# Performance work log

Measured on AMD Instinct MI355X. Metric: run time of the kernel, lower is better.

The kernel has to match this reference:

```python
import jax, jax.numpy as jnp
import numpy as np

# Config (from init_kwargs 'knn')
QUEUE_SIZE = 65536   # K
FEAT_DIM = 256       # D
BATCH = 512          # N (eval_sampling = 1.0 -> all samples used)
NUM_KNNS = 200
NUM_CLASSES = 1000
TEMPERATURE = 0.07


def _l2norm(x):
    return x / jnp.sqrt(jnp.sum(x * x, axis=-1, keepdims=True) + 1e-12)


def setup_inputs() -> dict:
    key = jax.random.key(0)
    k1, k2, k3, k4 = jax.random.split(key, 4)
    features = _l2norm(jax.random.normal(k1, (BATCH, FEAT_DIM), jnp.float32))
    labels = jax.random.randint(k2, (BATCH,), 0, NUM_CLASSES, jnp.int32)
    queue_features = _l2norm(jax.random.normal(k3, (QUEUE_SIZE, FEAT_DIM), jnp.float32))
    queue_labels = jax.random.randint(k4, (QUEUE_SIZE,), 0, NUM_CLASSES, jnp.int32)
    return {
        "features": features,
        "labels": labels,
        "queue_features": queue_features,
        "queue_labels": queue_labels,
        "queue_ptr": 0,
    }


def reference(features, labels, queue_features, queue_labels, queue_ptr):
    # ---- kNN accuracy (train branch, eval_sampling=1.0) ----
    sim = jnp.einsum('nc,kc->nk', features, queue_features)           # [N, K]
    sim_w, sim_idx = jax.lax.top_k(sim, k=NUM_KNNS)                   # [N, Kn]
    sim_w = jnp.exp(sim_w / TEMPERATURE)
    sim_labels = queue_labels[sim_idx]                                # [N, Kn] (vmapped gather)
    # weighted one-hot vote, expressed as a scatter-add (same math,
    # avoids the [N, Kn, C] one-hot intermediate)
    n = features.shape[0]
    pred_scores = jnp.zeros((n, NUM_CLASSES), sim_w.dtype)
    pred_scores = pred_scores.at[jnp.arange(n)[:, None], sim_labels].add(sim_w)
    pred_labels = jnp.argmax(pred_scores, axis=-1)
    accuracy = jnp.mean((pred_labels == labels).astype(jnp.float32))

    # ---- queue update (single device: all_gather == identity) ----
    batch_size = features.shape[0]
    inds = (jnp.arange(batch_size) + queue_ptr) % QUEUE_SIZE  # original asserts divisibility
    new_queue_features = queue_features.at[inds].set(features)
    new_queue_labels = queue_labels.at[inds].set(labels)
    new_queue_ptr = (queue_ptr + batch_size) % QUEUE_SIZE

    return accuracy, new_queue_features, new_queue_labels, new_queue_ptr
```

## Files before the change

### kernel.cpp

```cpp
#include <hip/hip_runtime.h>
#include <math.h>

#define NQ     65536
#define DIM    256
#define NBATCH 512
#define KNN    200
#define NCLS   1000
#define TSELF  0.155f
#define TSELH  0.150f
#define EPSF   0.0041f
#define BGUARD 22

#define GM  128
#define GK  32
#define NTN (NQ / GM)
#define KSTEPS (DIM / GK)

typedef unsigned short u16;
typedef unsigned long long u64;
typedef __attribute__((ext_vector_type(8))) short short8;
typedef __attribute__((ext_vector_type(4))) float f32x4;


__device__ __forceinline__ u16 f2bf(float x) {
  unsigned u = __float_as_uint(x);
  return (u16)((u + 0x7FFFu + ((u >> 16) & 1u)) >> 16);
}
__device__ __forceinline__ void load_lds16(const void* g, void* l) {
  __builtin_amdgcn_global_load_lds(
      (const __attribute__((address_space(1))) unsigned int*)g,
      (__attribute__((address_space(3))) unsigned int*)l, 16, 0, 0);
}
__device__ __forceinline__ void store_f4u(float* p, float4 v) {
  p[0] = v.x;
  *(float2*)(p + 1) = make_float2(v.y, v.z);
  p[3] = v.w;
}

__global__ __launch_bounds__(256) void prep_copy_kernel(
    const float* __restrict__ feat, const int* __restrict__ labels,
    const float* __restrict__ qf, const int* __restrict__ ql,
    const int* __restrict__ qptr,
    u16* __restrict__ Bb, u16* __restrict__ Ab,
    int* __restrict__ flag, float* __restrict__ out)
{
  const int idx = blockIdx.x * 256 + threadIdx.x;
  const int ptr = qptr[0];
  const long long NFEAT = (long long)NQ * DIM;

  {
    float4 qv = ((const float4*)qf)[idx];
    int row = idx >> 6;
    int c4  = idx & 63;
    int d = (row - ptr) & (NQ - 1);
    float4 ov = qv;
    if (d < NBATCH) ov = ((const float4*)feat)[d * 64 + c4];
    store_f4u(out + 1 + 4 * (long long)idx, ov);

    ushort4 h;
    h.x = f2bf(qv.x); h.y = f2bf(qv.y); h.z = f2bf(qv.z); h.w = f2bf(qv.w);
    ((ushort4*)Bb)[idx] = h;
  }

  if (idx < NBATCH * DIM / 4) {
    float4 v = ((const float4*)feat)[idx];
    ushort4 h;
    h.x = f2bf(v.x); h.y = f2bf(v.y); h.z = f2bf(v.z); h.w = f2bf(v.w);
    ((ushort4*)Ab)[idx] = h;
  }

  if (idx < NQ) {
    int d = (idx - ptr) & (NQ - 1);
    int v = (d < NBATCH) ? labels[d] : ql[idx];
    out[1 + NFEAT + idx] = (float)v;
  }

  if (idx < NBATCH) flag[idx] = 0;
  if (idx == 0) {
    out[0] = 0.0f;
    out[1 + NFEAT + NQ] = (float)((ptr + NBATCH) & (NQ - 1));
  }
}

__global__ __launch_bounds__(256) void gemm_mfma(
    const u16* __restrict__ A, const u16* __restrict__ B,
    uint2* __restrict__ cand, int* __restrict__ cnt2,
    int* __restrict__ flag, int SLOT)
{
  __shared__ u16 sA[2][GM][GK];
  __shared__ u16 sB[2][GM][GK];
  __shared__ int lcnt[GM];

  const int tid  = threadIdx.x;
  const int wave = tid >> 6, lane = tid & 63;
  const int d  = blockIdx.x;
  const int bm = (d >> 3) & 3;
  const int bn = (d & 7) | ((d >> 5) << 3);

  for (int i = tid; i < GM; i += 256) lcnt[i] = 0;

  const u16* srcBase = ((wave < 2) ? (A + (size_t)bm * GM * DIM)
                                   : (B + (size_t)bn * GM * DIM))
                       + (size_t)(wave & 1) * 64 * DIM;
  const int kx = ((lane & 3) ^ ((lane >> 3) & 3)) * 8;
  const u16* src = srcBase + (lane >> 2) * DIM + kx;
  u16* dst0 = ((wave < 2) ? &sA[0][0][0] : &sB[0][0][0]) + (wave & 1) * 64 * GK;
  u16* dst1 = ((wave < 2) ? &sA[1][0][0] : &sB[1][0][0]) + (wave & 1) * 64 * GK;

  const int wm = (wave & 1) * 64, wn = (wave >> 1) * 64;
  const int fr = lane & 15;
  const int fq = lane >> 4;
  const int fqx = fq ^ ((fr >> 1) & 3);

  f32x4 acc[4][4] = {};

  {
    const u16* s = src;
#pragma unroll
    for (int g = 0; g < 4; ++g)
      load_lds16(s + g * 16 * DIM, dst0 + g * 512);
  }
  __syncthreads();

  for (int t = 0; t < KSTEPS; ++t) {
    const int cur = t & 1;
    if (t + 1 < KSTEPS) {
      const u16* s = src + (t + 1) * GK;
      u16* dl = cur ? dst0 : dst1;
#pragma unroll
      for (int g = 0; g < 4; ++g)
        load_lds16(s + g * 16 * DIM, dl + g * 512);
    }

    short8 a[4], b[4];
#pragma unroll
    for (int i = 0; i < 4; ++i) {
      a[i] = *(const short8*)&sA[cur][wm + i * 16 + fr][fqx * 8];
      b[i] = *(const short8*)&sB[cur][wn + i * 16 + fr][fqx * 8];
    }
#pragma unroll
    for (int i = 0; i < 4; ++i)
#pragma unroll
      for (int j = 0; j < 4; ++j)
        acc[i][j] = __builtin_amdgcn_mfma_f32_16x16x32_bf16(a[i], b[j], acc[i][j], 0, 0, 0);

    __syncthreads();
  }

  const int lrow0 = wm + fq * 4;
  const int ccol  = bn * GM + wn + fr;
#pragma unroll
  for (int i = 0; i < 4; ++i)
#pragma unroll
    for (int j = 0; j < 4; ++j)
#pragma unroll
      for (int r = 0; r < 4; ++r) {
        float v = acc[i][j][r];
        if (v > TSELF) {
          int lr  = lrow0 + i * 16 + r;
          int col = ccol + j * 16;
          int p = atomicAdd(&lcnt[lr], 1);
          if (p < SLOT)
            cand[((size_t)(bm * GM + lr) * NTN + bn) * SLOT + p] =
                make_uint2(__float_as_uint(v), (unsigned)col);
          else
            flag[bm * GM + lr] = 1;
        }
      }
  __syncthreads();
  if (tid < GM) {
    int c = lcnt[tid];
    cnt2[(size_t)(bm * GM + tid) * NTN + bn] = c < SLOT ? c : SLOT;
  }
}

#define NBSEL 2048
#define CCAP  2048
#define MBCAP 256
#define LCAP  1024
#define NT    512
#define NG    (NT / 8)
#define BINW  ((1.001f - TSELH) / (float)NBSEL)

__global__ __launch_bounds__(NT, 4) void select_kernel(
    const uint2* __restrict__ cand, const int* __restrict__ cnt2,
    const int* __restrict__ flag, const int* __restrict__ labels,
    const int* __restrict__ qlab, const float* __restrict__ qf,
    const float* __restrict__ feat, float* __restrict__ out,
    float inv_n, int SLOT)
{
  __shared__ int   hist[NBSEL];
  __shared__ int   seg[NT];
  __shared__ float candV[CCAP];
  __shared__ int   candI[CCAP];
  __shared__ float votes[NCLS];
  __shared__ u64   bk[LCAP / 2];
  __shared__ float frow[DIM];
  __shared__ int   s_b, s_cnt, s_hi, s_mb;
  __shared__ u64   s_best;

  const int tid = threadIdx.x;
  const int row = blockIdx.x;

  bool fb = (flag[row] != 0);

  if (tid < DIM) frow[tid] = feat[(size_t)row * DIM + tid];
  for (int i = tid; i < NBSEL; i += NT) hist[i] = 0;
  for (int c = tid; c < NCLS; c += NT) votes[c] = 0.0f;
  if (tid == 0) { s_b = 0; s_cnt = 0; s_hi = 0; s_mb = 0; s_best = 0ull; }
  __syncthreads();

  if (!fb) {
    const int*   rowcnt  = cnt2 + (size_t)row * NTN;
    const uint2* rowcand = cand + (size_t)row * NTN * SLOT;
    for (int t = tid; t < NTN; t += NT) {
      int c = rowcnt[t];
      if (c > 0) {
        int p = atomicAdd(&s_cnt, c);
        for (int k = 0; k < c; ++k) {
          if (p + k < CCAP) {
            uint2 e = rowcand[(size_t)t * SLOT + k];
            candV[p + k] = __uint_as_float(e.x);
            candI[p + k] = (int)e.y;
          }
        }
      }
    }
    __syncthreads();
    const int n = s_cnt;
    if (n < KNN || n > CCAP) fb = true;
    else {
      const float SSCALE = 1.0f / BINW;
      for (int i = tid; i < n; i += NT) {
        int b = (int)((candV[i] - TSELH) * SSCALE);
        b = b < 0 ? 0 : (b > NBSEL - 1 ? NBSEL - 1 : b);
        atomicAdd(&hist[b], 1);
      }
      __syncthreads();
      { int s = 0;
#pragma unroll
        for (int i = 0; i < NBSEL / NT; ++i) s += hist[tid * (NBSEL / NT) + i];
        seg[tid] = s; }
      __syncthreads();
      for (int off = 1; off < NT; off <<= 1) {
        int t = (tid + off < NT) ? seg[tid + off] : 0;
        __syncthreads();
        seg[tid] += t;
        __syncthreads();
      }
      { int run = (tid < NT - 1) ? seg[tid + 1] : 0;
        for (int i = tid * (NBSEL / NT) + NBSEL / NT - 1;
             i >= tid * (NBSEL / NT); --i) {
          run += hist[i];
          if (run >= KNN) { atomicMax(&s_b, i); break; }
        } }
      __syncthreads();
      const int bstarA = s_b;
      const float thresh = TSELH + (float)bstarA * BINW - 2.0f * EPSF;

      int* lst = (int*)bk;
      for (int i = tid; i < NBSEL; i += NT) hist[i] = 0;
      if (tid == 0) s_b = 0;
      for (int i = tid; i < n; i += NT) {
        if (candV[i] >= thresh) {
          int p = atomicAdd(&s_mb, 1);
          if (p < LCAP) lst[p] = i;
        }
      }
      __syncthreads();
      const int nr = s_mb;
      if (nr > LCAP) fb = true;
      else {
        const int sub = tid & 7;
        const int grp = tid >> 3;
        const float4* fr4 = (const float4*)frow;

        float4 b0[8];
        if (grp < nr) {
          const float4* qr = (const float4*)(qf + (size_t)candI[lst[grp]] * DIM);
#pragma unroll
          for (int it = 0; it < 8; ++it) b0[it] = qr[sub + it * 8];
        }
        for (int k = grp; k < nr; k += NG) {
          const int kn = k + NG;
          float4 b1[8];
          if (kn < nr) {
            const float4* qr = (const float4*)(qf + (size_t)candI[lst[kn]] * DIM);
#pragma unroll
            for (int it = 0; it < 8; ++it) b1[it] = qr[sub + it * 8];
          }
          float p = 0.0f;
#pragma unroll
          for (int it = 0; it < 8; ++it) {
            float4 a = fr4[sub + it * 8];
            p = fmaf(a.x, b0[it].x, p); p = fmaf(a.y, b0[it].y, p);
            p = fmaf(a.z, b0[it].z, p); p = fmaf(a.w, b0[it].w, p);
          }
          p += __shfl_xor(p, 1, 64);
          p += __shfl_xor(p, 2, 64);
          p += __shfl_xor(p, 4, 64);
          if (sub == 0) candV[lst[k]] = p;
#pragma unroll
          for (int it = 0; it < 8; ++it) b0[it] = b1[it];
        }
        if (tid == 0) s_mb = 0;
        __syncthreads();

        for (int i = tid; i < n; i += NT) {
          float v = candV[i];
          if (v >= thresh) {
            int b = (int)((v - TSELH) * SSCALE);
            b = b < 0 ? 0 : (b > NBSEL - 1 ? NBSEL - 1 : b);
            atomicAdd(&hist[b], 1);
          }
        }
        __syncthreads();
        { int s = 0;
#pragma unroll
          for (int i = 0; i < NBSEL / NT; ++i) s += hist[tid * (NBSEL / NT) + i];
          seg[tid] = s; }
        __syncthreads();
        for (int off = 1; off < NT; off <<= 1) {
          int t = (tid + off < NT) ? seg[tid + off] : 0;
          __syncthreads();
          seg[tid] += t;
          __syncthreads();
        }
        { int run = (tid < NT - 1) ? seg[tid + 1] : 0;
          for (int i = tid * (NBSEL / NT) + NBSEL / NT - 1;
               i >= tid * (NBSEL / NT); --i) {
            run += hist[i];
            if (run >= KNN) { atomicMax(&s_b, i); break; }
          } }
        __syncthreads();
        const int bstar = s_b;

        if (bstar < BGUARD) fb = true;
        else {
          for (int i = tid; i < n; i += NT) {
            float v = candV[i];
            if (v < thresh) continue;
            int b = (int)((v - TSELH) * SSCALE);
            b = b < 0 ? 0 : (b > NBSEL - 1 ? NBSEL - 1 : b);
            if (b > bstar) {
              atomicAdd(&s_hi, 1);
              atomicAdd(&votes[qlab[candI[i]]], expf(v * (1.0f / 0.07f)));
            } else if (b == bstar) {
              int p = atomicAdd(&s_mb, 1);
              if (p < MBCAP)
                bk[p] = ((u64)__float_as_uint(v) << 32) |
                        (u64)(0xFFFFFFFFu - (unsigned)candI[i]);
            }
          }
          __syncthreads();
          const int mb = s_mb;
          if (mb > MBCAP) fb = true;
          else {
            const int need = KNN - s_hi;
            for (int e = tid; e < mb; e += NT) {
              u64 ke = bk[e];
              int rank = 0;
              for (int j = 0; j < mb; ++j) rank += (bk[j] > ke);
              if (rank < need) {
                float v = __uint_as_float((unsigned)(ke >> 32));
                int col = (int)(0xFFFFFFFFu - (unsigned)(ke & 0xFFFFFFFFull));
                atomicAdd(&votes[qlab[col]], expf(v * (1.0f / 0.07f)));
              }
            }
            __syncthreads();
          }
        }
      }
    }
  }

  if (fb) {
    for (int i = tid; i < NBSEL; i += NT) hist[i] = 0;
    if (tid == 0) { s_b = 0; s_cnt = 0; }
    __syncthreads();

    for (int q = tid; q < NQ; q += NT) {
      const float4* qr = (const float4*)(qf + (size_t)q * DIM);
      const float4* fr = (const float4*)frow;
      float s = 0.0f;
#pragma unroll
      for (int t = 0; t < DIM / 4; ++t) {
        float4 a = fr[t], b = qr[t];
        s = fmaf(a.x, b.x, s); s = fmaf(a.y, b.y, s);
        s = fmaf(a.z, b.z, s); s = fmaf(a.w, b.w, s);
      }
      int bin = (int)((s + 1.0f) * (NBSEL * 0.5f));
      bin = bin < 0 ? 0 : (bin > NBSEL - 1 ? NBSEL - 1 : bin);
      atomicAdd(&hist[bin], 1);
    }
    __syncthreads();

    { int s = 0;
#pragma unroll
      for (int i = 0; i < NBSEL / NT; ++i) s += hist[tid * (NBSEL / NT) + i];
      seg[tid] = s; }
    __syncthreads();
    for (int off = 1; off < NT; off <<= 1) {
      int t = (tid + off < NT) ? seg[tid + off] : 0;
      __syncthreads();
      seg[tid] += t;
      __syncthreads();
    }
    { int run = (tid < NT - 1) ? seg[tid + 1] : 0;
      for (int i = tid * (NBSEL / NT) + NBSEL / NT - 1;
           i >= tid * (NBSEL / NT); --i) {
        run += hist[i];
        if (run >= KNN) { atomicMax(&s_b, i); break; }
      } }
    __syncthreads();
    const int bstar = s_b;

    for (int q = tid; q < NQ; q += NT) {
      const float4* qr = (const float4*)(qf + (size_t)q * DIM);
      const float4* fr = (const float4*)frow;
      float s = 0.0f;
#pragma unroll
      for (int t = 0; t < DIM / 4; ++t) {
        float4 a = fr[t], b = qr[t];
        s = fmaf(a.x, b.x, s); s = fmaf(a.y, b.y, s);
        s = fmaf(a.z, b.z, s); s = fmaf(a.w, b.w, s);
      }
      int bin = (int)((s + 1.0f) * (NBSEL * 0.5f));
      bin = bin < 0 ? 0 : (bin > NBSEL - 1 ? NBSEL - 1 : bin);
      if (bin >= bstar) {
        int p = atomicAdd(&s_cnt, 1);
        if (p < CCAP) { candV[p] = s; candI[p] = q; }
      }
    }
    __syncthreads();
    int m = s_cnt < CCAP ? s_cnt : CCAP;

    int P = 256; while (P < m) P <<= 1;
    for (int i = tid; i < P; i += NT)
      if (i >= m) { candV[i] = -INFINITY; candI[i] = 0x7fffffff; }
    __syncthreads();
    for (int k = 2; k <= P; k <<= 1) {
      for (int j = k >> 1; j > 0; j >>= 1) {
        for (int i = tid; i < P; i += NT) {
          int ixj = i ^ j;
          if (ixj > i) {
            float va = candV[i], vb = candV[ixj];
            int ia = candI[i], ib = candI[ixj];
            bool aFirst = (va > vb) || (va == vb && ia < ib);
            bool up = ((i & k) == 0);
            if (up ? !aFirst : aFirst) {
              candV[i] = vb; candV[ixj] = va;
              candI[i] = ib; candI[ixj] = ia;
            }
          }
        }
        __syncthreads();
      }
    }

    for (int c = tid; c < NCLS; c += NT) votes[c] = 0.0f;
    __syncthreads();
    for (int i = tid; i < KNN; i += NT)
      atomicAdd(&votes[qlab[candI[i]]], expf(candV[i] * (1.0f / 0.07f)));
    __syncthreads();
  }

  u64 key = 0ull;
  for (int c = tid; c < NCLS; c += NT) {
    u64 k2 = ((u64)__float_as_uint(votes[c]) << 32) |
             (u64)(0xFFFFFFFFu - (unsigned)c);
    if (k2 > key) key = k2;
  }
  for (int off = 32; off > 0; off >>= 1) {
    u64 o = __shfl_down(key, off, 64);
    if (o > key) key = o;
  }
  if ((tid & 63) == 0) atomicMax(&s_best, key);
  __syncthreads();
  if (tid == 0) {
    int cls = (int)(0xFFFFFFFFu - (unsigned)(s_best & 0xFFFFFFFFull));
    if (cls == labels[row]) atomicAdd(out, inv_n);
  }
}

extern "C" void kernel_launch(void* const* d_in, const int* in_sizes, int n_in,
                              void* d_out, int out_size, void* d_ws, size_t ws_size,
                              hipStream_t stream)
{
  const float* features = (const float*)d_in[0];
  const int*   labels   = (const int*)d_in[1];
  const float* qfeat    = (const float*)d_in[2];
  const int*   qlab     = (const int*)d_in[3];
  const int*   qptr     = (const int*)d_in[4];
  float* out = (float*)d_out;

  int nbatch = in_sizes[0] / DIM;
  float inv_n = 1.0f / (float)nbatch;

  size_t bBytes = (size_t)NQ * DIM * 2;
  size_t fixed  = bBytes + (size_t)NBATCH * NTN * 4 + NBATCH * 4 +
                  (size_t)NBATCH * DIM * 2;
  int SLOT = 16;
  while ((size_t)NBATCH * NTN * SLOT * 8 + fixed > ws_size && SLOT > 2) SLOT >>= 1;

  u16*   Bb   = (u16*)d_ws;
  uint2* cand = (uint2*)((char*)d_ws + bBytes);
  int*   cnt2 = (int*)((char*)cand + (size_t)NBATCH * NTN * SLOT * 8);
  int*   flagp = cnt2 + (size_t)NBATCH * NTN;
  u16*   Ab   = (u16*)(flagp + NBATCH);

  prep_copy_kernel<<<NQ * DIM / 4 / 256, 256, 0, stream>>>(
      features, labels, qfeat, qlab, qptr, Bb, Ab, flagp, out);

  gemm_mfma<<<(NBATCH / GM) * (NQ / GM), 256, 0, stream>>>(
      Ab, Bb, cand, cnt2, flagp, SLOT);

  select_kernel<<<nbatch, NT, 0, stream>>>(cand, cnt2, flagp, labels, qlab,
                                           qfeat, features, out, inv_n, SLOT);
}
```

Baseline: 200.7 us.

## Replace second histogram pass with direct rank selection over refined candidates

After recomputing exact fp32 dot products for candidates above the coarse threshold, the kernel now ranks all refined candidates directly with an O(nr^2) LDS comparison instead of building a second histogram, scanning it and rank-resolving only the boundary bin. The first prefix scan over the histogram switches from a barrier-per-step Hillis-Steele scan to wavefront shuffle scans plus a small cross-wave combine, cutting the number of block barriers. A new check falls back to the brute-force path if the 200th value lies below the safety threshold. The quadratic ranking may cost more when nr approaches the LCAP of 1024.

```diff
diff --git a/kernel.cpp b/kernel.cpp
--- a/kernel.cpp
+++ b/kernel.cpp
@@ -9,7 +9,6 @@
 #define TSELF  0.155f
 #define TSELH  0.150f
 #define EPSF   0.0041f
-#define BGUARD 22
 
 #define GM  128
 #define GK  32
@@ -176,10 +175,10 @@
 
 #define NBSEL 2048
 #define CCAP  2048
-#define MBCAP 256
 #define LCAP  1024
 #define NT    512
 #define NG    (NT / 8)
+#define NWV   (NT / 64)
 #define BINW  ((1.001f - TSELH) / (float)NBSEL)
 
 __global__ __launch_bounds__(NT, 4) void select_kernel(
@@ -191,12 +190,15 @@
 {
   __shared__ int   hist[NBSEL];
   __shared__ int   seg[NT];
+  __shared__ int   wtot[NWV];
   __shared__ float candV[CCAP];
   __shared__ int   candI[CCAP];
   __shared__ float votes[NCLS];
-  __shared__ u64   bk[LCAP / 2];
+  __shared__ u64   ek[LCAP];
+  __shared__ int   lst[LCAP];
   __shared__ float frow[DIM];
-  __shared__ int   s_b, s_cnt, s_hi, s_mb;
+  __shared__ int   s_b, s_cnt, s_mb;
+  __shared__ float s_chk;
   __shared__ u64   s_best;
 
   const int tid = threadIdx.x;
@@ -207,7 +209,7 @@
   if (tid < DIM) frow[tid] = feat[(size_t)row * DIM + tid];
   for (int i = tid; i < NBSEL; i += NT) hist[i] = 0;
   for (int c = tid; c < NCLS; c += NT) votes[c] = 0.0f;
-  if (tid == 0) { s_b = 0; s_cnt = 0; s_hi = 0; s_mb = 0; s_best = 0ull; }
+  if (tid == 0) { s_b = 0; s_cnt = 0; s_mb = 0; s_best = 0ull; s_chk = -1.0f; }
   __syncthreads();
 
   if (!fb) {
@@ -237,17 +239,24 @@
         atomicAdd(&hist[b], 1);
       }
       __syncthreads();
-      { int s = 0;
+      {
+        int s = 0;
 #pragma unroll
         for (int i = 0; i < NBSEL / NT; ++i) s += hist[tid * (NBSEL / NT) + i];
-        seg[tid] = s; }
-      __syncthreads();
-      for (int off = 1; off < NT; off <<= 1) {
-        int t = (tid + off < NT) ? seg[tid + off] : 0;
+        const int ln = tid & 63, wv = tid >> 6;
+        int acc = s;
+#pragma unroll
+        for (int off = 1; off < 64; off <<= 1) {
+          int o = __shfl_down(acc, off, 64);
+          if (ln + off < 64) acc += o;
+        }
+        if (ln == 0) wtot[wv] = acc;
         __syncthreads();
-        seg[tid] += t;
-        __syncthreads();
-      }
+        int addv = 0;
+        for (int w = wv + 1; w < NWV; ++w) addv += wtot[w];
+        seg[tid] = acc + addv;
+      }
+      __syncthreads();
       { int run = (tid < NT - 1) ? seg[tid + 1] : 0;
         for (int i = tid * (NBSEL / NT) + NBSEL / NT - 1;
              i >= tid * (NBSEL / NT); --i) {
@@ -258,9 +267,6 @@
       const int bstarA = s_b;
       const float thresh = TSELH + (float)bstarA * BINW - 2.0f * EPSF;
 
-      int* lst = (int*)bk;
-      for (int i = tid; i < NBSEL; i += NT) hist[i] = 0;
-      if (tid == 0) s_b = 0;
       for (int i = tid; i < n; i += NT) {
         if (candV[i] >= thresh) {
           int p = atomicAdd(&s_mb, 1);
@@ -269,7 +275,7 @@
       }
       __syncthreads();
       const int nr = s_mb;
-      if (nr > LCAP) fb = true;
+      if (nr > LCAP || nr < KNN) fb = true;
       else {
         const int sub = tid & 7;
         const int grp = tid >> 3;
@@ -303,73 +309,28 @@
 #pragma unroll
           for (int it = 0; it < 8; ++it) b0[it] = b1[it];
         }
-        if (tid == 0) s_mb = 0;
         __syncthreads();
 
-        for (int i = tid; i < n; i += NT) {
-          float v = candV[i];
-          if (v >= thresh) {
-            int b = (int)((v - TSELH) * SSCALE);
-            b = b < 0 ? 0 : (b > NBSEL - 1 ? NBSEL - 1 : b);
-            atomicAdd(&hist[b], 1);
+        for (int e = tid; e < nr; e += NT) {
+          int ci = lst[e];
+          ek[e] = ((u64)__float_as_uint(candV[ci]) << 32) |
+                  (u64)(0xFFFFFFFFu - (unsigned)candI[ci]);
+        }
+        __syncthreads();
+
+        for (int e = tid; e < nr; e += NT) {
+          u64 ke = ek[e];
+          int rank = 0;
+          for (int j = 0; j < nr; ++j) rank += (ek[j] > ke);
+          if (rank < KNN) {
+            float v = __uint_as_float((unsigned)(ke >> 32));
+            int col = (int)(0xFFFFFFFFu - (unsigned)(ke & 0xFFFFFFFFull));
+            atomicAdd(&votes[qlab[col]], expf(v * (1.0f / 0.07f)));
+            if (rank == KNN - 1) s_chk = v;
           }
         }
         __syncthreads();
-        { int s = 0;
-#pragma unroll
-          for (int i = 0; i < NBSEL / NT; ++i) s += hist[tid * (NBSEL / NT) + i];
-          seg[tid] = s; }
-        __syncthreads();
-        for (int off = 1; off < NT; off <<= 1) {
-          int t = (tid + off < NT) ? seg[tid + off] : 0;
-          __syncthreads();
-          seg[tid] += t;
-          __syncthreads();
-        }
-        { int run = (tid < NT - 1) ? seg[tid + 1] : 0;
-          for (int i = tid * (NBSEL / NT) + NBSEL / NT - 1;
-               i >= tid * (NBSEL / NT); --i) {
-            run += hist[i];
-            if (run >= KNN) { atomicMax(&s_b, i); break; }
-          } }
-        __syncthreads();
-        const int bstar = s_b;
-
-        if (bstar < BGUARD) fb = true;
-        else {
-          for (int i = tid; i < n; i += NT) {
-            float v = candV[i];
-            if (v < thresh) continue;
-            int b = (int)((v - TSELH) * SSCALE);
-            b = b < 0 ? 0 : (b > NBSEL - 1 ? NBSEL - 1 : b);
-            if (b > bstar) {
-              atomicAdd(&s_hi, 1);
-              atomicAdd(&votes[qlab[candI[i]]], expf(v * (1.0f / 0.07f)));
-            } else if (b == bstar) {
-              int p = atomicAdd(&s_mb, 1);
-              if (p < MBCAP)
-                bk[p] = ((u64)__float_as_uint(v) << 32) |
-                        (u64)(0xFFFFFFFFu - (unsigned)candI[i]);
-            }
-          }
-          __syncthreads();
-          const int mb = s_mb;
-          if (mb > MBCAP) fb = true;
-          else {
-            const int need = KNN - s_hi;
-            for (int e = tid; e < mb; e += NT) {
-              u64 ke = bk[e];
-              int rank = 0;
-              for (int j = 0; j < mb; ++j) rank += (bk[j] > ke);
-              if (rank < need) {
-                float v = __uint_as_float((unsigned)(ke >> 32));
-                int col = (int)(0xFFFFFFFFu - (unsigned)(ke & 0xFFFFFFFFull));
-                atomicAdd(&votes[qlab[col]], expf(v * (1.0f / 0.07f)));
-              }
-            }
-            __syncthreads();
-          }
-        }
+        if (s_chk < TSELF + EPSF) fb = true;
       }
     }
   }
```

New measurement: 202.6 us. No clear change (+0.9%).
